# Performance work log

Measured on AMD Instinct MI355X. Metric: run time of the kernel, lower is better.

## Reference

```python
import jax, jax.numpy as jnp
import numpy as np
import math

# dims
B, L, D = 2, 2048, 1024          # batch, seq len, embedding_dim
HID, ATT, H = 1024, 512, 8       # linear_hidden_dim, attention_dim, num_heads
DQK, DUV = ATT // H, HID // H    # 64, 128
NBUCK = 64                       # time_num_buckets
MAX_SPAN = 86400 * 90            # max_time_span
EPS = 1e-6
OUT_DIM = 2 * HID + 2 * ATT      # uvqk output dim = 3072


def _time_boundaries():
    # RelativeAttentionBiasModule._build_boundaries: pure log buckets
    steps = NBUCK - 1
    log_part = np.exp(np.linspace(0.0, math.log(MAX_SPAN), steps))
    b = np.unique(np.floor(np.clip(log_part, 1, None)).astype(np.int64)).astype(np.float32)
    return jnp.asarray(b)

_BOUNDARIES = _time_boundaries()  # len <= 63, indices < NBUCK


def setup_inputs() -> dict:
    key = jax.random.key(0)
    ks = jax.random.split(key, 8)
    x = jax.random.normal(ks[0], (B, L, D), dtype=jnp.float32)
    timestamps = jnp.sort(
        jax.random.randint(ks[1], (B, L), 0, 2592000), axis=-1
    )  # chronological event times (seconds)
    attn_mask = jnp.tril(jnp.ones((L, L), dtype=bool))[None].repeat(B, axis=0)  # causal
    W_uvqk = jax.random.normal(ks[2], (OUT_DIM, D), dtype=jnp.float32) * 0.02
    b_uvqk = jnp.zeros((OUT_DIM,), dtype=jnp.float32)
    time_bias = jax.random.normal(ks[3], (NBUCK, H), dtype=jnp.float32) * 0.02
    W_o = jax.random.normal(ks[4], (D, HID), dtype=jnp.float32) * 0.02
    b_o = jnp.zeros((D,), dtype=jnp.float32)
    rms_w = jnp.ones((HID,), dtype=jnp.float32)
    return {"x": x, "timestamps": timestamps, "attn_mask": attn_mask,
            "W_uvqk": W_uvqk, "b_uvqk": b_uvqk, "time_bias": time_bias,
            "W_o": W_o, "b_o": b_o, "rms_w": rms_w}


def reference(x, timestamps, attn_mask, W_uvqk, b_uvqk, time_bias, W_o, b_o, rms_w):
    Bx, Lx, _ = x.shape
    scale = 1.0 / math.sqrt(DQK)

    # fused uvqk projection + act1 (silu)
    h = jax.nn.silu(x @ W_uvqk.T + b_uvqk)  # [B, L, OUT_DIM]
    u, v, q, k = jnp.split(h, [HID, 2 * HID, 2 * HID + ATT], axis=-1)

    def heads(t, d):  # [B, L, H*d] -> [B, H, L, d]
        return t.reshape(Bx, Lx, H, d).transpose(0, 2, 1, 3)

    u = heads(u, DUV)
    v = heads(v, DUV)
    q = heads(q, DQK) * scale
    k = heads(k, DQK)

    logits = jnp.einsum('bhid,bhjd->bhij', q.astype(jnp.float32), k.astype(jnp.float32))

    # bucketized relative-time bias (per-head)
    tdiff = jnp.abs(timestamps[:, :, None] - timestamps[:, None, :])
    tdiff = jnp.clip(tdiff, 1, None).astype(jnp.float32)  # clamp_min(1)
    bk = jnp.searchsorted(_BOUNDARIES, tdiff, side='left')  # torch.bucketize right=False
    rab = time_bias[bk].transpose(0, 3, 1, 2)  # [B, H, L, L]

    # pointwise silu attention (no softmax), masked
    A = jax.nn.silu(logits + rab) * attn_mask[:, None].astype(jnp.float32)

    y = jnp.einsum('bhij,bhjd->bhid', A, v)               # [B, H, L, DUV]
    y = y.transpose(0, 2, 1, 3).reshape(Bx, Lx, HID)       # merge heads
    u_m = u.transpose(0, 2, 1, 3).reshape(Bx, Lx, HID)

    # RMSNorm then U-gate
    rms = y * jax.lax.rsqrt(jnp.mean(y * y, axis=-1, keepdims=True) + EPS) * rms_w
    y_point = rms.astype(x.dtype) * u_m

    return y_point @ W_o.T + b_o  # [B, L, D]
```

## Files before the change

### kernel.cpp

```cpp
#include <hip/hip_runtime.h>
#include <hip/hip_bf16.h>

typedef float f32x4 __attribute__((ext_vector_type(4)));
typedef short s16x8 __attribute__((ext_vector_type(8)));
typedef short s16x4 __attribute__((ext_vector_type(4)));
typedef unsigned short u16x4 __attribute__((ext_vector_type(4)));

__device__ __forceinline__ float bf2f(unsigned short u) {
    union { unsigned int i; float f; } x; x.i = ((unsigned int)u) << 16; return x.f;
}
__device__ __forceinline__ unsigned short f2bf(float f) {
    union { float f; unsigned int i; } x; x.f = f;
    unsigned int r = x.i + 0x7FFFu + ((x.i >> 16) & 1u);
    return (unsigned short)(r >> 16);
}
__device__ __forceinline__ float silu(float v) {
    return v / (1.f + __expf(-v));
}
__device__ __forceinline__ float silu_fast(float v) {
    return v * __builtin_amdgcn_rcpf(1.f + __expf(-v));
}

#define GLDS16(gp, lp) __builtin_amdgcn_global_load_lds( \
    (const __attribute__((address_space(1))) unsigned int*)(gp), \
    (__attribute__((address_space(3))) unsigned int*)(lp), 16, 0, 0)

__global__ __launch_bounds__(256) void cvt_bf16(
    const float* __restrict__ X, const float* __restrict__ W,
    const float* __restrict__ Wo,
    unsigned short* __restrict__ Xb, unsigned short* __restrict__ Wb,
    unsigned short* __restrict__ Wob)
{
    int idx = blockIdx.x * 256 + threadIdx.x;
    const float* src; unsigned short* dst; int off;
    if (idx < 1048576)       { src = X;  dst = Xb;  off = idx; }
    else if (idx < 1835008)  { src = W;  dst = Wb;  off = idx - 1048576; }
    else                     { src = Wo; dst = Wob; off = idx - 1835008; }
    f32x4 v = *reinterpret_cast<const f32x4*>(&src[(size_t)off * 4]);
    u16x4 o;
    #pragma unroll
    for (int j = 0; j < 4; ++j) o[j] = f2bf(v[j]);
    *reinterpret_cast<u16x4*>(&dst[(size_t)off * 4]) = o;
}

__global__ __launch_bounds__(256) void bucketize(
    const int* __restrict__ TS, unsigned char* __restrict__ BK)
{
    const int jt = blockIdx.x, it = blockIdx.y, b = blockIdx.z;
    if (jt > it) return;
    __shared__ int bndRaw[63];
    __shared__ int bnd[64];
    __shared__ int tsi[64], tsj[64];
    const int tid = threadIdx.x;
    if (tid < 63) {
        double step = log(7776000.0) / 62.0;
        double v = exp(step * (double)tid);
        if (v < 1.0) v = 1.0;
        bndRaw[tid] = (int)floor(v);
    }
    if (tid >= 64 && tid < 128) tsi[tid - 64] = TS[b * 2048 + it * 64 + (tid - 64)];
    else if (tid >= 128 && tid < 192) tsj[tid - 128] = TS[b * 2048 + jt * 64 + (tid - 128)];
    __syncthreads();
    if (tid == 0) {
        int c = 0, p = -1;
        for (int i = 0; i < 63; ++i) { int x = bndRaw[i]; if (x != p) { bnd[c++] = x; p = x; } }
        for (; c < 64; ++c) bnd[c] = 0x7FFFFFFF;
    }
    __syncthreads();
    const int il = tid & 63, jc = (tid >> 6) * 16;
    const int tiv = tsi[il];
    unsigned char out[16];
    #pragma unroll
    for (int u = 0; u < 16; ++u) {
        int td = tiv - tsj[jc + u]; td = td < 0 ? -td : td; if (td < 1) td = 1;
        int pos = 0;
        #pragma unroll
        for (int st = 32; st; st >>= 1)
            if (bnd[pos + st - 1] < td) pos += st;
        out[u] = (unsigned char)pos;
    }
    *reinterpret_cast<int4*>(&BK[((size_t)b << 22) + (size_t)(it * 64 + il) * 2048 + jt * 64 + jc]) =
        *reinterpret_cast<const int4*>(out);
}

__global__ __launch_bounds__(256) void gemm_uvqk(
    const unsigned short* __restrict__ Xb, const unsigned short* __restrict__ Wb,
    const float* __restrict__ bias,
    unsigned short* __restrict__ U, unsigned short* __restrict__ Vt,
    unsigned short* __restrict__ Q, unsigned short* __restrict__ K)
{
    __shared__ __align__(16) unsigned short smem[2][128][64];
    const int tid = threadIdx.x;
    const int wv = tid >> 6, lane = tid & 63;
    const int g = lane >> 4, lr = lane & 15;
    const int wid = (blockIdx.x & 7) * 96 + (blockIdx.x >> 3);
    const int m0 = (wid & 31) * 128, n0 = (wid >> 5) * 128;
    const int wr = (wv >> 1) * 64, wc = (wv & 1) * 64;
    const int ls = lr & 7;
    f32x4 acc[4][4] = {};

    for (int k0 = 0; k0 < 1024; k0 += 64) {
        #pragma unroll
        for (int c = 0; c < 4; ++c) {
            int id = c * 256 + tid;
            int row = id >> 3, c8 = id & 7;
            int sc = (c8 ^ (row & 7)) * 8;
            GLDS16(&Xb[(size_t)(m0 + row) * 1024 + k0 + sc], &smem[0][row][c8 * 8]);
            GLDS16(&Wb[(size_t)(n0 + row) * 1024 + k0 + sc], &smem[1][row][c8 * 8]);
        }
        __syncthreads();
        s16x8 afr[4][2], bfr[4][2];
        #pragma unroll
        for (int i = 0; i < 4; ++i)
            #pragma unroll
            for (int kq = 0; kq < 2; ++kq) {
                afr[i][kq] = *reinterpret_cast<const s16x8*>(
                    &smem[0][wr + i * 16 + lr][((kq * 4 + g) ^ ls) * 8]);
                bfr[i][kq] = *reinterpret_cast<const s16x8*>(
                    &smem[1][wc + i * 16 + lr][((kq * 4 + g) ^ ls) * 8]);
            }
        #pragma unroll
        for (int kq = 0; kq < 2; ++kq)
            #pragma unroll
            for (int mi = 0; mi < 4; ++mi)
                #pragma unroll
                for (int ni = 0; ni < 4; ++ni)
                    acc[mi][ni] = __builtin_amdgcn_mfma_f32_16x16x32_bf16(
                        afr[mi][kq], bfr[ni][kq], acc[mi][ni], 0, 0, 0);
        __syncthreads();
    }

    if (n0 >= 1024 && n0 < 2048) {
        const int head = (n0 - 1024) >> 7;
        unsigned short* sT = &smem[0][0][0] + wv * (32 * 72);
        #pragma unroll
        for (int hh = 0; hh < 2; ++hh) {
            #pragma unroll
            for (int nn = 0; nn < 2; ++nn) {
                int ni = hh * 2 + nn;
                float bn = bias[n0 + wc + ni * 16 + lr];
                #pragma unroll
                for (int mi = 0; mi < 4; ++mi)
                    #pragma unroll
                    for (int r = 0; r < 4; ++r)
                        sT[(nn * 16 + lr) * 72 + mi * 16 + g * 4 + r] =
                            f2bf(silu(acc[mi][ni][r] + bn));
            }
            #pragma unroll
            for (int c = 0; c < 4; ++c) {
                int id = c * 64 + lane;
                int row = id >> 3, ch = id & 7;
                s16x8 val = *reinterpret_cast<const s16x8*>(&sT[row * 72 + ch * 8]);
                int d = wc + hh * 32 + row;
                int mg = m0 + wr + ch * 8;
                int bb = mg >> 11, l = mg & 2047;
                *reinterpret_cast<s16x8*>(
                    &Vt[(((size_t)(bb * 8 + head) * 128 + d) << 11) + l]) = val;
            }
        }
    } else {
        #pragma unroll
        for (int ni = 0; ni < 4; ++ni) {
            int n = n0 + wc + ni * 16 + lr;
            float bn = bias[n];
            #pragma unroll
            for (int mi = 0; mi < 4; ++mi) {
                #pragma unroll
                for (int r = 0; r < 4; ++r) {
                    int m = m0 + wr + mi * 16 + g * 4 + r;
                    float v = silu(acc[mi][ni][r] + bn);
                    int b = m >> 11, l = m & 2047;
                    if (n < 1024) {
                        U[(size_t)m * 1024 + n] = f2bf(v);
                    } else if (n < 2560) {
                        int dd = n - 2048, h = dd >> 6, d = dd & 63;
                        Q[((((size_t)(b * 8 + h) << 11) + l) << 6) + d] = f2bf(v * 0.125f);
                    } else {
                        int dd = n - 2560, h = dd >> 6, d = dd & 63;
                        K[((((size_t)(b * 8 + h) << 11) + l) << 6) + d] = f2bf(v);
                    }
                }
            }
        }
    }
}

__global__ __launch_bounds__(512, 1) void attn(
    const unsigned short* __restrict__ Q, const unsigned short* __restrict__ K,
    const unsigned short* __restrict__ Vt, const unsigned char* __restrict__ BK,
    const float* __restrict__ TB, float* __restrict__ Y)
{
    __shared__ __align__(16) unsigned short sK[2][2][64][64];
    __shared__ __align__(16) unsigned short sV[2][2][128][64];
    __shared__ __align__(16) unsigned char  sBK[2][2][64][64];

    const int tid = threadIdx.x, wv = tid >> 6, lane = tid & 63;
    const int g = lane >> 4, lr = lane & 15;

    const int bid = blockIdx.x;
    const int xcd = bid & 7, kix = bid >> 3;
    const int bh = 2 * xcd + (kix & 1);
    const int ti = 31 - (kix >> 1);
    const int b = bh >> 3, h = bh & 7;
    const int i0 = ti * 64;
    const int rg = wv & 3;
    const int half = wv >> 2;
    const int irow = i0 + rg * 16;
    const int P = (ti + 2) >> 1;

    const int tbl = __float_as_int(TB[lane * 8 + h]);

    const unsigned short* qb = Q + ((size_t)bh << 11) * 64;
    const unsigned short* kb = K + ((size_t)bh << 11) * 64;
    const unsigned short* vtb = Vt + ((size_t)bh << 7) * 2048;
    const unsigned char* bkb = BK + ((size_t)b << 22);

    s16x8 aq[2];
    #pragma unroll
    for (int kq = 0; kq < 2; ++kq)
        aq[kq] = *reinterpret_cast<const s16x8*>(&qb[(size_t)(irow + lr) * 64 + kq * 32 + g * 8]);

    char* sKb = (char*)&sK[0][0][0][0];
    char* sVb = (char*)&sV[0][0][0][0];
    char* sBKb = (char*)&sBK[0][0][0][0];
    const int cs = lr & 7;
    const int ib = irow + lr;

    auto stage = [&](int q, int db) {
        int jth = 2 * q + half;
        if (jth > ti) jth = 2 * q;
        const size_t j0 = (size_t)jth * 64;
        char* kd = sKb + db * 16384 + half * 8192;
        char* vd = sVb + db * 32768 + half * 16384;
        char* bkd = sBKb + db * 8192 + half * 4096;
        #pragma unroll
        for (int c = 0; c < 2; ++c) {
            int chunk = rg * 128 + c * 64 + lane;
            int row = chunk >> 3, c8 = chunk & 7;
            GLDS16(kb + (j0 + row) * 64 + ((c8 ^ (row & 7)) * 8), kd + chunk * 16);
        }
        #pragma unroll
        for (int c = 0; c < 4; ++c) {
            int chunk = rg * 256 + c * 64 + lane;
            int d = chunk >> 3, c8 = chunk & 7;
            GLDS16(vtb + (size_t)d * 2048 + j0 + ((c8 ^ (d & 7)) * 8), vd + chunk * 16);
        }
        {
            int chunk = rg * 64 + lane;
            int row = chunk >> 2, c16 = chunk & 3;
            GLDS16(bkb + (size_t)(i0 + row) * 2048 + j0 + ((c16 ^ (row & 3)) * 16), bkd + chunk * 16);
        }
    };

    f32x4 accy[8] = {};

#define COMPUTE(DB) { \
        const int jt = 2 * p + half; \
        if (jt <= ti) { \
            const char* kbase = sKb + (DB) * 16384 + half * 8192; \
            f32x4 sacc[4] = {}; \
            _Pragma("unroll") \
            for (int ni = 0; ni < 4; ++ni) { \
                _Pragma("unroll") \
                for (int kq = 0; kq < 2; ++kq) { \
                    s16x8 kf = *reinterpret_cast<const s16x8*>( \
                        kbase + (ni * 16 + lr) * 128 + (((kq * 4 + g) ^ cs) << 4)); \
                    sacc[ni] = __builtin_amdgcn_mfma_f32_16x16x32_bf16(kf, aq[kq], sacc[ni], 0, 0, 0); \
                } \
            } \
            const int j0 = jt * 64; \
            const bool diag = (jt == ti); \
            s16x4 pf[4]; \
            _Pragma("unroll") \
            for (int ni = 0; ni < 4; ++ni) { \
                unsigned int bw = *reinterpret_cast<const unsigned int*>( \
                    sBKb + (DB) * 8192 + half * 4096 + (rg * 16 + lr) * 64 + ((ni ^ (lr & 3)) << 4) + g * 4); \
                float b0 = __int_as_float(__builtin_amdgcn_ds_bpermute((int)((bw & 255u) << 2), tbl)); \
                float b1 = __int_as_float(__builtin_amdgcn_ds_bpermute((int)(((bw >> 8) & 255u) << 2), tbl)); \
                float b2 = __int_as_float(__builtin_amdgcn_ds_bpermute((int)(((bw >> 16) & 255u) << 2), tbl)); \
                float b3 = __int_as_float(__builtin_amdgcn_ds_bpermute((int)((bw >> 24) << 2), tbl)); \
                float v0 = silu_fast(sacc[ni][0] + b0); \
                float v1 = silu_fast(sacc[ni][1] + b1); \
                float v2 = silu_fast(sacc[ni][2] + b2); \
                float v3 = silu_fast(sacc[ni][3] + b3); \
                if (diag) { \
                    int jb = j0 + ni * 16 + g * 4; \
                    if (jb + 0 > ib) v0 = 0.f; \
                    if (jb + 1 > ib) v1 = 0.f; \
                    if (jb + 2 > ib) v2 = 0.f; \
                    if (jb + 3 > ib) v3 = 0.f; \
                } \
                unsigned int w0, w1; \
                asm("v_cvt_pk_bf16_f32 %0, %1, %2" : "=v"(w0) : "v"(v0), "v"(v1)); \
                asm("v_cvt_pk_bf16_f32 %0, %1, %2" : "=v"(w1) : "v"(v2), "v"(v3)); \
                union { unsigned int u_[2]; s16x4 v_; } cvt_; \
                cvt_.u_[0] = w0; cvt_.u_[1] = w1; \
                pf[ni] = cvt_.v_; \
            } \
            const char* vbase = sVb + (DB) * 32768 + half * 16384; \
            _Pragma("unroll") \
            for (int di = 0; di < 8; ++di) { \
                _Pragma("unroll") \
                for (int ni = 0; ni < 4; ++ni) { \
                    s16x4 vf = *reinterpret_cast<const s16x4*>( \
                        vbase + (di * 16 + lr) * 128 + (((2 * ni + (g >> 1)) ^ cs) << 4) + ((g & 1) << 3)); \
                    accy[di] = __builtin_amdgcn_mfma_f32_16x16x16bf16_1k(pf[ni], vf, accy[di], 0, 0, 0); \
                } \
            } \
        } }

    stage(0, 0);

    int p = 0;
    for (;;) {
        __builtin_amdgcn_s_barrier();
        if (p + 1 < P) {
            stage(p + 1, 1);
            asm volatile("s_waitcnt vmcnt(7)" ::: "memory");
        } else {
            asm volatile("s_waitcnt vmcnt(0)" ::: "memory");
        }
        __builtin_amdgcn_s_barrier();
        COMPUTE(0);
        if (++p == P) break;
        __builtin_amdgcn_s_barrier();
        if (p + 1 < P) {
            stage(p + 1, 0);
            asm volatile("s_waitcnt vmcnt(7)" ::: "memory");
        } else {
            asm volatile("s_waitcnt vmcnt(0)" ::: "memory");
        }
        __builtin_amdgcn_s_barrier();
        COMPUTE(1);
        if (++p == P) break;
    }
#undef COMPUTE

    __syncthreads();
    float* red = (float*)sVb;
    if (wv >= 4) {
        #pragma unroll
        for (int di = 0; di < 8; ++di)
            #pragma unroll
            for (int r = 0; r < 4; ++r)
                red[(rg * 16 + g * 4 + r) * 132 + di * 16 + lr] = accy[di][r];
    }
    __syncthreads();
    if (wv < 4) {
        #pragma unroll
        for (int di = 0; di < 8; ++di)
            #pragma unroll
            for (int r = 0; r < 4; ++r) {
                float s = accy[di][r] + red[(rg * 16 + g * 4 + r) * 132 + di * 16 + lr];
                Y[(size_t)((b << 11) + irow + g * 4 + r) * 1024 + h * 128 + di * 16 + lr] = s;
            }
    }
}

__global__ __launch_bounds__(256) void rmsnorm_gate(
    const float* __restrict__ Y, const unsigned short* __restrict__ U,
    const float* __restrict__ rw, unsigned short* __restrict__ YP)
{
    __shared__ float red[4];
    const int row = blockIdx.x, tid = threadIdx.x;
    f32x4 v = *reinterpret_cast<const f32x4*>(&Y[(size_t)row * 1024 + tid * 4]);
    float ss = v[0] * v[0] + v[1] * v[1] + v[2] * v[2] + v[3] * v[3];
    #pragma unroll
    for (int off = 32; off; off >>= 1) ss += __shfl_down(ss, off);
    if ((tid & 63) == 0) red[tid >> 6] = ss;
    __syncthreads();
    float rms = rsqrtf((red[0] + red[1] + red[2] + red[3]) * (1.f / 1024.f) + 1e-6f);
    #pragma unroll
    for (int j = 0; j < 4; ++j) {
        int c = tid * 4 + j;
        float o = v[j] * rms * rw[c] * bf2f(U[(size_t)row * 1024 + c]);
        YP[(size_t)row * 1024 + c] = f2bf(o);
    }
}

__global__ __launch_bounds__(512) void gemm_out(
    const unsigned short* __restrict__ YP, const unsigned short* __restrict__ Wob,
    const float* __restrict__ bo, float* __restrict__ OUT)
{
    __shared__ __align__(16) unsigned short sA[128][64];
    __shared__ __align__(16) unsigned short sB[128][64];
    const int tid = threadIdx.x;
    const int wv = tid >> 6, lane = tid & 63;
    const int g = lane >> 4, lr = lane & 15;
    const int wid = (blockIdx.x & 7) * 32 + (blockIdx.x >> 3);
    const int m0 = (wid & 31) * 128, n0 = (wid >> 5) * 128;
    const int wr = (wv >> 2) * 64, wc = (wv & 3) * 32;
    const int ls = lr & 7;
    f32x4 acc[4][2] = {};

    for (int k0 = 0; k0 < 1024; k0 += 64) {
        #pragma unroll
        for (int c = 0; c < 2; ++c) {
            int id = c * 512 + tid;
            int row = id >> 3, c8 = id & 7;
            int sc = (c8 ^ (row & 7)) * 8;
            GLDS16(&YP[(size_t)(m0 + row) * 1024 + k0 + sc], &sA[row][c8 * 8]);
            GLDS16(&Wob[(size_t)(n0 + row) * 1024 + k0 + sc], &sB[row][c8 * 8]);
        }
        __syncthreads();
        s16x8 afr[4][2], bfr[2][2];
        #pragma unroll
        for (int kq = 0; kq < 2; ++kq) {
            #pragma unroll
            for (int i = 0; i < 4; ++i)
                afr[i][kq] = *reinterpret_cast<const s16x8*>(
                    &sA[wr + i * 16 + lr][((kq * 4 + g) ^ ls) * 8]);
            #pragma unroll
            for (int i = 0; i < 2; ++i)
                bfr[i][kq] = *reinterpret_cast<const s16x8*>(
                    &sB[wc + i * 16 + lr][((kq * 4 + g) ^ ls) * 8]);
        }
        #pragma unroll
        for (int kq = 0; kq < 2; ++kq)
            #pragma unroll
            for (int mi = 0; mi < 4; ++mi)
                #pragma unroll
                for (int ni = 0; ni < 2; ++ni)
                    acc[mi][ni] = __builtin_amdgcn_mfma_f32_16x16x32_bf16(
                        afr[mi][kq], bfr[ni][kq], acc[mi][ni], 0, 0, 0);
        __syncthreads();
    }

    #pragma unroll
    for (int ni = 0; ni < 2; ++ni) {
        int n = n0 + wc + ni * 16 + lr;
        float bn = bo[n];
        #pragma unroll
        for (int mi = 0; mi < 4; ++mi)
            #pragma unroll
            for (int r = 0; r < 4; ++r) {
                int m = m0 + wr + mi * 16 + g * 4 + r;
                OUT[(size_t)m * 1024 + n] = acc[mi][ni][r] + bn;
            }
    }
}

extern "C" void kernel_launch(void* const* d_in, const int* in_sizes, int n_in,
                              void* d_out, int out_size, void* d_ws, size_t ws_size,
                              hipStream_t stream) {
    const float* X     = (const float*)d_in[0];
    const int*   TS    = (const int*)d_in[1];
    const float* Wuvqk = (const float*)d_in[3];
    const float* buvqk = (const float*)d_in[4];
    const float* TB    = (const float*)d_in[5];
    const float* Wo    = (const float*)d_in[6];
    const float* bo    = (const float*)d_in[7];
    const float* rw    = (const float*)d_in[8];
    float* OUT = (float*)d_out;

    char* ws = (char*)d_ws;
    unsigned short* Qb  = (unsigned short*)(ws);
    unsigned short* Kb  = (unsigned short*)(ws + (4u << 20));
    unsigned short* Vt  = (unsigned short*)(ws + (8u << 20));
    unsigned short* Ub  = (unsigned short*)(ws + (16u << 20));
    float*          Yb  = (float*)(ws + (24u << 20));
    unsigned short* Xb  = (unsigned short*)(ws + (24u << 20));
    unsigned short* Wb  = (unsigned short*)(ws + (32u << 20));
    unsigned short* YP  = (unsigned short*)(ws + (40u << 20));
    unsigned char*  BKm = (unsigned char*)(ws + (48u << 20));
    unsigned short* Wob = (unsigned short*)(ws + (56u << 20));

    cvt_bf16<<<8192, 256, 0, stream>>>(X, Wuvqk, Wo, Xb, Wb, Wob);
    bucketize<<<dim3(32, 32, 2), 256, 0, stream>>>(TS, BKm);
    gemm_uvqk<<<768, 256, 0, stream>>>(Xb, Wb, buvqk, Ub, Vt, Qb, Kb);
    attn<<<512, 512, 0, stream>>>(Qb, Kb, Vt, BKm, TB, Yb);
    rmsnorm_gate<<<4096, 256, 0, stream>>>(Yb, Ub, rw, YP);
    gemm_out<<<256, 512, 0, stream>>>(YP, Wob, bo, OUT);
}
```

Measured before the change: 149.7 us.

## Double-buffer LDS in projection GEMMs with prefetch and fine-grained waits

Both GEMM kernels (uvqk projection and output projection) now use two LDS buffers with a K-step of 32 instead of one buffer with a K-step of 64. The next tile is prefetched via global_load_lds while the current one is consumed, using explicit vmcnt waits and raw barriers instead of __syncthreads. The XOR swizzle is dropped, which may cause LDS bank conflicts on 64-byte rows. The epilogue also switches silu to a fast-reciprocal variant.

```diff
diff --git a/kernel.cpp b/kernel.cpp
--- a/kernel.cpp
+++ b/kernel.cpp
@@ -89,50 +89,57 @@
     unsigned short* __restrict__ U, unsigned short* __restrict__ Vt,
     unsigned short* __restrict__ Q, unsigned short* __restrict__ K)
 {
-    __shared__ __align__(16) unsigned short smem[2][128][64];
+    __shared__ __align__(16) unsigned short sA[2][128][32];
+    __shared__ __align__(16) unsigned short sB[2][128][32];
     const int tid = threadIdx.x;
     const int wv = tid >> 6, lane = tid & 63;
     const int g = lane >> 4, lr = lane & 15;
     const int wid = (blockIdx.x & 7) * 96 + (blockIdx.x >> 3);
     const int m0 = (wid & 31) * 128, n0 = (wid >> 5) * 128;
     const int wr = (wv >> 1) * 64, wc = (wv & 1) * 64;
-    const int ls = lr & 7;
+    const int srow = tid >> 2, sc8 = (tid & 3) * 8;
     f32x4 acc[4][4] = {};
 
-    for (int k0 = 0; k0 < 1024; k0 += 64) {
-        #pragma unroll
-        for (int c = 0; c < 4; ++c) {
-            int id = c * 256 + tid;
-            int row = id >> 3, c8 = id & 7;
-            int sc = (c8 ^ (row & 7)) * 8;
-            GLDS16(&Xb[(size_t)(m0 + row) * 1024 + k0 + sc], &smem[0][row][c8 * 8]);
-            GLDS16(&Wb[(size_t)(n0 + row) * 1024 + k0 + sc], &smem[1][row][c8 * 8]);
-        }
-        __syncthreads();
-        s16x8 afr[4][2], bfr[4][2];
+    auto stage = [&](int kt, int db) {
+        const int k0 = kt * 32;
+        #pragma unroll
+        for (int c = 0; c < 2; ++c) {
+            int row = srow + c * 64;
+            GLDS16(&Xb[(size_t)(m0 + row) * 1024 + k0 + sc8], &sA[db][row][sc8]);
+            GLDS16(&Wb[(size_t)(n0 + row) * 1024 + k0 + sc8], &sB[db][row][sc8]);
+        }
+    };
+
+    stage(0, 0);
+    for (int kt = 0; kt < 32; ++kt) {
+        const int db = kt & 1;
+        __builtin_amdgcn_s_barrier();
+        if (kt < 31) {
+            stage(kt + 1, db ^ 1);
+            asm volatile("s_waitcnt vmcnt(4)" ::: "memory");
+        } else {
+            asm volatile("s_waitcnt vmcnt(0)" ::: "memory");
+        }
+        __builtin_amdgcn_s_barrier();
+        s16x8 afr[4], bfr[4];
         #pragma unroll
         for (int i = 0; i < 4; ++i)
-            #pragma unroll
-            for (int kq = 0; kq < 2; ++kq) {
-                afr[i][kq] = *reinterpret_cast<const s16x8*>(
-                    &smem[0][wr + i * 16 + lr][((kq * 4 + g) ^ ls) * 8]);
-                bfr[i][kq] = *reinterpret_cast<const s16x8*>(
-                    &smem[1][wc + i * 16 + lr][((kq * 4 + g) ^ ls) * 8]);
-            }
-        #pragma unroll
-        for (int kq = 0; kq < 2; ++kq)
-            #pragma unroll
-            for (int mi = 0; mi < 4; ++mi)
-                #pragma unroll
-                for (int ni = 0; ni < 4; ++ni)
-                    acc[mi][ni] = __builtin_amdgcn_mfma_f32_16x16x32_bf16(
-                        afr[mi][kq], bfr[ni][kq], acc[mi][ni], 0, 0, 0);
-        __syncthreads();
-    }
+            afr[i] = *reinterpret_cast<const s16x8*>(&sA[db][wr + i * 16 + lr][g * 8]);
+        #pragma unroll
+        for (int i = 0; i < 4; ++i)
+            bfr[i] = *reinterpret_cast<const s16x8*>(&sB[db][wc + i * 16 + lr][g * 8]);
+        #pragma unroll
+        for (int mi = 0; mi < 4; ++mi)
+            #pragma unroll
+            for (int ni = 0; ni < 4; ++ni)
+                acc[mi][ni] = __builtin_amdgcn_mfma_f32_16x16x32_bf16(
+                    afr[mi], bfr[ni], acc[mi][ni], 0, 0, 0);
+    }
+    __builtin_amdgcn_s_barrier();
 
     if (n0 >= 1024 && n0 < 2048) {
         const int head = (n0 - 1024) >> 7;
-        unsigned short* sT = &smem[0][0][0] + wv * (32 * 72);
+        unsigned short* sT = &sA[0][0][0] + wv * (32 * 72);
         #pragma unroll
         for (int hh = 0; hh < 2; ++hh) {
             #pragma unroll
@@ -144,7 +151,7 @@
                     #pragma unroll
                     for (int r = 0; r < 4; ++r)
                         sT[(nn * 16 + lr) * 72 + mi * 16 + g * 4 + r] =
-                            f2bf(silu(acc[mi][ni][r] + bn));
+                            f2bf(silu_fast(acc[mi][ni][r] + bn));
             }
             #pragma unroll
             for (int c = 0; c < 4; ++c) {
@@ -168,7 +175,7 @@
                 #pragma unroll
                 for (int r = 0; r < 4; ++r) {
                     int m = m0 + wr + mi * 16 + g * 4 + r;
-                    float v = silu(acc[mi][ni][r] + bn);
+                    float v = silu_fast(acc[mi][ni][r] + bn);
                     int b = m >> 11, l = m & 2047;
                     if (n < 1024) {
                         U[(size_t)m * 1024 + n] = f2bf(v);
@@ -382,48 +389,47 @@
     const unsigned short* __restrict__ YP, const unsigned short* __restrict__ Wob,
     const float* __restrict__ bo, float* __restrict__ OUT)
 {
-    __shared__ __align__(16) unsigned short sA[128][64];
-    __shared__ __align__(16) unsigned short sB[128][64];
+    __shared__ __align__(16) unsigned short sA[2][128][32];
+    __shared__ __align__(16) unsigned short sB[2][128][32];
     const int tid = threadIdx.x;
     const int wv = tid >> 6, lane = tid & 63;
     const int g = lane >> 4, lr = lane & 15;
     const int wid = (blockIdx.x & 7) * 32 + (blockIdx.x >> 3);
     const int m0 = (wid & 31) * 128, n0 = (wid >> 5) * 128;
     const int wr = (wv >> 2) * 64, wc = (wv & 3) * 32;
-    const int ls = lr & 7;
+    const int srow = tid >> 2, sc8 = (tid & 3) * 8;
     f32x4 acc[4][2] = {};
 
-    for (int k0 = 0; k0 < 1024; k0 += 64) {
-        #pragma unroll
-        for (int c = 0; c < 2; ++c) {
-            int id = c * 512 + tid;
-            int row = id >> 3, c8 = id & 7;
-            int sc = (c8 ^ (row & 7)) * 8;
-            GLDS16(&YP[(size_t)(m0 + row) * 1024 + k0 + sc], &sA[row][c8 * 8]);
-            GLDS16(&Wob[(size_t)(n0 + row) * 1024 + k0 + sc], &sB[row][c8 * 8]);
-        }
-        __syncthreads();
-        s16x8 afr[4][2], bfr[2][2];
-        #pragma unroll
-        for (int kq = 0; kq < 2; ++kq) {
-            #pragma unroll
-            for (int i = 0; i < 4; ++i)
-                afr[i][kq] = *reinterpret_cast<const s16x8*>(
-                    &sA[wr + i * 16 + lr][((kq * 4 + g) ^ ls) * 8]);
-            #pragma unroll
-            for (int i = 0; i < 2; ++i)
-                bfr[i][kq] = *reinterpret_cast<const s16x8*>(
-                    &sB[wc + i * 16 + lr][((kq * 4 + g) ^ ls) * 8]);
-        }
-        #pragma unroll
-        for (int kq = 0; kq < 2; ++kq)
-            #pragma unroll
-            for (int mi = 0; mi < 4; ++mi)
-                #pragma unroll
-                for (int ni = 0; ni < 2; ++ni)
-                    acc[mi][ni] = __builtin_amdgcn_mfma_f32_16x16x32_bf16(
-                        afr[mi][kq], bfr[ni][kq], acc[mi][ni], 0, 0, 0);
-        __syncthreads();
+    auto stage = [&](int kt, int db) {
+        const int k0 = kt * 32;
+        GLDS16(&YP[(size_t)(m0 + srow) * 1024 + k0 + sc8], &sA[db][srow][sc8]);
+        GLDS16(&Wob[(size_t)(n0 + srow) * 1024 + k0 + sc8], &sB[db][srow][sc8]);
+    };
+
+    stage(0, 0);
+    for (int kt = 0; kt < 32; ++kt) {
+        const int db = kt & 1;
+        __builtin_amdgcn_s_barrier();
+        if (kt < 31) {
+            stage(kt + 1, db ^ 1);
+            asm volatile("s_waitcnt vmcnt(2)" ::: "memory");
+        } else {
+            asm volatile("s_waitcnt vmcnt(0)" ::: "memory");
+        }
+        __builtin_amdgcn_s_barrier();
+        s16x8 afr[4], bfr[2];
+        #pragma unroll
+        for (int i = 0; i < 4; ++i)
+            afr[i] = *reinterpret_cast<const s16x8*>(&sA[db][wr + i * 16 + lr][g * 8]);
+        #pragma unroll
+        for (int i = 0; i < 2; ++i)
+            bfr[i] = *reinterpret_cast<const s16x8*>(&sB[db][wc + i * 16 + lr][g * 8]);
+        #pragma unroll
+        for (int mi = 0; mi < 4; ++mi)
+            #pragma unroll
+            for (int ni = 0; ni < 2; ++ni)
+                acc[mi][ni] = __builtin_amdgcn_mfma_f32_16x16x32_bf16(
+                    afr[mi], bfr[ni], acc[mi][ni], 0, 0, 0);
     }
 
     #pragma unroll
```

After: 157.4 us. 5.1% more time.
